# Performance work log

Hardware: AMD Instinct MI355X
Metric: run time of the kernel (lower is better)

Reference implementation:

```python
import jax, jax.numpy as jnp
import numpy as np

H = 512   # span_encoder_hidden_dim == input dim (required by the slicing in forward)
L = 128   # sequence length
B = 4     # batch size


def setup_inputs() -> dict:
    key = jax.random.key(0)
    ks = jax.random.split(key, 7)
    s = 1.0 / np.sqrt(H)
    u = lambda k, shape: jax.random.uniform(k, shape, jnp.float32, -s, s)
    return {
        "word_repr": jax.random.normal(ks[0], (B, L, H), jnp.float32),
        "W_ih_f": u(ks[1], (4 * H, H)),
        "W_hh_f": u(ks[2], (4 * H, H)),
        "b_f": u(ks[3], (4 * H,)),
        "W_ih_b": u(ks[4], (4 * H, H)),
        "W_hh_b": u(ks[5], (4 * H, H)),
        "b_b": u(ks[6], (4 * H,)),
    }


def _lstm(xs, W_ih, W_hh, b):
    # xs: (T, B, D) -> hidden states (T, B, H). PyTorch gate order: i, f, g, o.
    bsz = xs.shape[1]
    hdim = W_hh.shape[1]
    h0 = jnp.zeros((bsz, hdim), xs.dtype)

    def step(carry, xt):
        h, c = carry
        g = xt @ W_ih.T + h @ W_hh.T + b
        gi, gf, gg, go = jnp.split(g, 4, axis=-1)
        c = jax.nn.sigmoid(gf) * c + jax.nn.sigmoid(gi) * jnp.tanh(gg)
        h = jax.nn.sigmoid(go) * jnp.tanh(c)
        return (h, c), h

    _, hs = jax.lax.scan(step, (h0, h0), xs)
    return hs


def reference(word_repr, W_ih_f, W_hh_f, b_f, W_ih_b, W_hh_b, b_b):
    bsz, length, dim = word_repr.shape
    z = jnp.zeros((bsz, 1, dim), word_repr.dtype)
    x = jnp.concatenate([z, word_repr, z], axis=1)      # (B, L+2, D) zero-padded
    xs = jnp.swapaxes(x, 0, 1)                          # (T=L+2, B, D)
    hf = _lstm(xs, W_ih_f, W_hh_f, b_f)                 # forward direction (T, B, H)
    hb = _lstm(xs[::-1], W_ih_b, W_hh_b, b_b)[::-1]     # backward direction (T, B, H)

    Fl = hf[:length]           # forward_repr at positions 0..L-1, (L, B, H)
    Bl = hb[1:length + 1]      # backward_repr at positions 1..L,  (L, B, H)

    # r[i, k] = concat(F[k] - F[i], Bk = B[i+1] - B[k+1]) — fully broadcast, no python loop
    diff_f = Fl[None, :] - Fl[:, None]     # (L, L, B, H)
    diff_b = Bl[:, None] - Bl[None, :]     # (L, L, B, H)
    r = jnp.concatenate([diff_f, diff_b], axis=-1)  # (L, L, B, 2H)

    # original only fills i in [1, L-2], k in [i+1, L-2]; zero elsewhere (torch.empty -> defined zeros)
    ii = jnp.arange(length)[:, None]
    kk = jnp.arange(length)[None, :]
    valid = (ii >= 1) & (kk > ii) & (kk <= length - 2)
    return jnp.where(valid[:, :, None, None], r, jnp.zeros((), r.dtype))
```

## Files before the change

### kernel.cpp

```cpp
#include <hip/hip_runtime.h>
#include <math.h>

#define HH 512
#define LL 128
#define BB 4
#define TT 130
#define G4 2048

#define HF_OFF 0
#define HB_OFF 268288
#define CNT_OFF 536576
#define XPROJ_PER_DIR (TT * BB * G4)
#define XPROJ_OFF (67108864 - 2 * XPROJ_PER_DIR)

__global__ __launch_bounds__(256) void k0_init(float* ws) {
    int tid = threadIdx.x;
    float* HF = ws + HF_OFF;
    float* HB = ws + HB_OFF;
    int* cnt = (int*)(ws + CNT_OFF);
    for (int i = tid; i < G4; i += 256) {
        HF[i] = 0.f;
        HB[(size_t)TT * G4 + i] = 0.f;
    }
    for (int i = tid; i < 2 * 131; i += 256) cnt[i] = 0;
}

__global__ __launch_bounds__(256) void k1_xproj(
    const float* __restrict__ wr,
    const float* __restrict__ WihF, const float* __restrict__ bF,
    const float* __restrict__ WihB, const float* __restrict__ bB,
    float* __restrict__ outbuf) {
    __shared__ float As[16][132];
    __shared__ float Bs[16][132];
    int bid = blockIdx.x;
    int d = bid / 80;
    int r2 = bid % 80;
    int mt = r2 >> 4, nt = r2 & 15;
    const float* Wih  = d ? WihB : WihF;
    const float* bias = d ? bB : bF;
    float* xp = outbuf + XPROJ_OFF + (size_t)d * XPROJ_PER_DIR;
    int tid = threadIdx.x;
    int ty = tid >> 4, tx = tid & 15;
    int m0 = mt * 128, n0 = nt * 128;

    float acc[8][8];
#pragma unroll
    for (int i = 0; i < 8; i++)
#pragma unroll
        for (int j = 0; j < 8; j++) acc[i][j] = 0.f;

    for (int k0 = 0; k0 < HH; k0 += 16) {
#pragma unroll
        for (int l = tid; l < 512; l += 256) {
            int rrow = l & 127;
            int kq = l >> 7;
            int m = m0 + rrow;
            int t = m >> 2, b = m & 3;
            float4 av = make_float4(0.f, 0.f, 0.f, 0.f);
            if (t >= 1 && t <= 128)
                av = *(const float4*)&wr[((size_t)b * LL + (t - 1)) * HH + k0 + kq * 4];
            As[kq * 4 + 0][rrow] = av.x;
            As[kq * 4 + 1][rrow] = av.y;
            As[kq * 4 + 2][rrow] = av.z;
            As[kq * 4 + 3][rrow] = av.w;
            float4 bv = *(const float4*)&Wih[(size_t)(n0 + rrow) * HH + k0 + kq * 4];
            Bs[kq * 4 + 0][rrow] = bv.x;
            Bs[kq * 4 + 1][rrow] = bv.y;
            Bs[kq * 4 + 2][rrow] = bv.z;
            Bs[kq * 4 + 3][rrow] = bv.w;
        }
        __syncthreads();
#pragma unroll
        for (int kk = 0; kk < 16; kk++) {
            float4 a0 = *(const float4*)&As[kk][ty * 8];
            float4 a1 = *(const float4*)&As[kk][ty * 8 + 4];
            float4 b0 = *(const float4*)&Bs[kk][tx * 8];
            float4 b1 = *(const float4*)&Bs[kk][tx * 8 + 4];
            float am[8] = {a0.x, a0.y, a0.z, a0.w, a1.x, a1.y, a1.z, a1.w};
            float bn[8] = {b0.x, b0.y, b0.z, b0.w, b1.x, b1.y, b1.z, b1.w};
#pragma unroll
            for (int i = 0; i < 8; i++)
#pragma unroll
                for (int j = 0; j < 8; j++) acc[i][j] = fmaf(am[i], bn[j], acc[i][j]);
        }
        __syncthreads();
    }
    float4 bv0 = *(const float4*)&bias[n0 + tx * 8];
    float4 bv1 = *(const float4*)&bias[n0 + tx * 8 + 4];
#pragma unroll
    for (int i = 0; i < 8; i++) {
        int m = m0 + ty * 8 + i;
        if (m < TT * BB) {
            float4 o0 = make_float4(acc[i][0] + bv0.x, acc[i][1] + bv0.y,
                                    acc[i][2] + bv0.z, acc[i][3] + bv0.w);
            float4 o1 = make_float4(acc[i][4] + bv1.x, acc[i][5] + bv1.y,
                                    acc[i][6] + bv1.z, acc[i][7] + bv1.w);
            *(float4*)&xp[(size_t)m * G4 + n0 + tx * 8] = o0;
            *(float4*)&xp[(size_t)m * G4 + n0 + tx * 8 + 4] = o1;
        }
    }
}

__device__ __forceinline__ float sigm_(float x) { return 1.f / (1.f + __expf(-x)); }
__device__ __forceinline__ float tanh_(float x) {
    float xc = fminf(fmaxf(x, -15.f), 15.f);
    float e = __expf(-2.f * xc);
    return (1.f - e) / (1.f + e);
}

__global__ __launch_bounds__(256, 1) void k2_lstm(
    const float* __restrict__ WhhF, const float* __restrict__ WhhB,
    const float* __restrict__ outbuf, float* __restrict__ ws) {
    __shared__ float4 hlds4[512];
    __shared__ float g_lds[64][4];
    __shared__ float clds[16][4];

    int bid = blockIdx.x;
    int dir = bid >> 5;
    int g = bid & 31;
    int j0 = g * 16;
    const float* Whh = dir ? WhhB : WhhF;
    const float* xp = outbuf + XPROJ_OFF + (size_t)dir * XPROJ_PER_DIR;
    float* Hbase = ws + (dir ? HB_OFF : HF_OFF);
    int* cnt = (int*)(ws + CNT_OFF) + dir * 131;
    int tid = threadIdx.x;
    int rg = tid >> 5, cc = tid & 31;

    float w[8][16];
#pragma unroll
    for (int i = 0; i < 8; i++) {
        int rl = rg * 8 + i;
        int q = rl >> 4, u = rl & 15;
        const float* wrow = Whh + (size_t)(q * 512 + j0 + u) * HH + cc * 16;
#pragma unroll
        for (int c4 = 0; c4 < 4; c4++) {
            float4 v = *(const float4*)&wrow[c4 * 4];
            w[i][c4 * 4 + 0] = v.x;
            w[i][c4 * 4 + 1] = v.y;
            w[i][c4 * 4 + 2] = v.z;
            w[i][c4 * 4 + 3] = v.w;
        }
    }

    int u_ = (tid >> 2) & 15, b_ = tid & 3;

    for (int s = 0; s < TT; s++) {
        int t = dir ? (129 - s) : s;
        int slot_in = dir ? (t + 1) : t;
        int slot_out = dir ? t : (t + 1);

        float xq[4] = {0.f, 0.f, 0.f, 0.f};
        if (tid < 64) {
#pragma unroll
            for (int q = 0; q < 4; q++)
                xq[q] = xp[((size_t)t * BB + b_) * G4 + q * 512 + j0 + u_];
        }

        if (s > 0) {
            if (tid == 0) {
                while (__hip_atomic_load(&cnt[slot_in], __ATOMIC_RELAXED,
                                         __HIP_MEMORY_SCOPE_AGENT) < 32) {}
            }
            __syncthreads();
            __threadfence();
        }

        const float4* hsrc = (const float4*)(Hbase + (size_t)slot_in * G4);
#pragma unroll
        for (int l = tid; l < 512; l += 256) {
            int brow = l >> 7;
            int quad = l & 127;
            int qs = quad ^ ((quad >> 2) & 7);
            hlds4[brow * 128 + qs] = hsrc[l];
        }
        __syncthreads();

        float p[8][4];
#pragma unroll
        for (int i = 0; i < 8; i++)
#pragma unroll
            for (int b = 0; b < 4; b++) p[i][b] = 0.f;
#pragma unroll
        for (int b = 0; b < 4; b++) {
#pragma unroll
            for (int c4 = 0; c4 < 4; c4++) {
                int quad = cc * 4 + c4;
                int qs = quad ^ (cc & 7);
                float4 h4 = hlds4[b * 128 + qs];
#pragma unroll
                for (int i = 0; i < 8; i++) {
                    p[i][b] = fmaf(w[i][c4 * 4 + 0], h4.x, p[i][b]);
                    p[i][b] = fmaf(w[i][c4 * 4 + 1], h4.y, p[i][b]);
                    p[i][b] = fmaf(w[i][c4 * 4 + 2], h4.z, p[i][b]);
                    p[i][b] = fmaf(w[i][c4 * 4 + 3], h4.w, p[i][b]);
                }
            }
        }
#pragma unroll
        for (int m = 1; m < 32; m <<= 1) {
#pragma unroll
            for (int i = 0; i < 8; i++)
#pragma unroll
                for (int b = 0; b < 4; b++) p[i][b] += __shfl_xor(p[i][b], m, 64);
        }
        if (cc == 0) {
#pragma unroll
            for (int i = 0; i < 8; i++)
#pragma unroll
                for (int b = 0; b < 4; b++) g_lds[rg * 8 + i][b] = p[i][b];
        }
        __syncthreads();

        if (tid < 64) {
            float gv[4];
#pragma unroll
            for (int q = 0; q < 4; q++) gv[q] = g_lds[q * 16 + u_][b_] + xq[q];
            float cprev = (s == 0) ? 0.f : clds[u_][b_];
            float si = sigm_(gv[0]);
            float sf = sigm_(gv[1]);
            float tg = tanh_(gv[2]);
            float so = sigm_(gv[3]);
            float cn = sf * cprev + si * tg;
            clds[u_][b_] = cn;
            Hbase[(size_t)slot_out * G4 + b_ * HH + j0 + u_] = so * tanh_(cn);
        }
        __syncthreads();
        if (tid == 0) {
            __threadfence();
            __hip_atomic_fetch_add(&cnt[slot_out], 1, __ATOMIC_RELEASE,
                                   __HIP_MEMORY_SCOPE_AGENT);
        }
    }
}

__global__ __launch_bounds__(256) void k3_out(const float* __restrict__ ws,
                                              float* __restrict__ out) {
    const float* HF = ws + HF_OFF;
    const float* HB = ws + HB_OFF;
    size_t idx = (size_t)blockIdx.x * 256 + threadIdx.x;
    const size_t total = 16777216;
    const size_t stride = (size_t)2048 * 256;
    for (; idx < total; idx += stride) {
        int c4 = idx & 255;
        int b = (idx >> 8) & 3;
        int k = (idx >> 10) & 127;
        int i = (int)(idx >> 17);
        float4 res = make_float4(0.f, 0.f, 0.f, 0.f);
        if (i >= 1 && k > i && k <= 126) {
            int c0 = c4 * 4;
            if (c0 < 512) {
                float4 a = *(const float4*)&HF[(size_t)(k + 1) * G4 + b * HH + c0];
                float4 c = *(const float4*)&HF[(size_t)(i + 1) * G4 + b * HH + c0];
                res = make_float4(a.x - c.x, a.y - c.y, a.z - c.z, a.w - c.w);
            } else {
                int cd = c0 - 512;
                float4 a = *(const float4*)&HB[(size_t)(i + 1) * G4 + b * HH + cd];
                float4 c = *(const float4*)&HB[(size_t)(k + 1) * G4 + b * HH + cd];
                res = make_float4(a.x - c.x, a.y - c.y, a.z - c.z, a.w - c.w);
            }
        }
        *(float4*)&out[idx * 4] = res;
    }
}

extern "C" void kernel_launch(void* const* d_in, const int* in_sizes, int n_in,
                              void* d_out, int out_size, void* d_ws, size_t ws_size,
                              hipStream_t stream) {
    const float* wr   = (const float*)d_in[0];
    const float* WihF = (const float*)d_in[1];
    const float* WhhF = (const float*)d_in[2];
    const float* bF   = (const float*)d_in[3];
    const float* WihB = (const float*)d_in[4];
    const float* WhhB = (const float*)d_in[5];
    const float* bB   = (const float*)d_in[6];
    float* out = (float*)d_out;
    float* ws = (float*)d_ws;

    k0_init<<<1, 256, 0, stream>>>(ws);
    k1_xproj<<<160, 256, 0, stream>>>(wr, WihF, bF, WihB, bB, out);
    k2_lstm<<<64, 256, 0, stream>>>(WhhF, WhhB, out, ws);
    k3_out<<<2048, 256, 0, stream>>>(ws, out);
}
```

Baseline: 1.678 ms.

## Lighten LSTM recurrence sync, use transpose-reduce, nontemporal output stores

The persistent recurrent kernel drops the __threadfence calls and one __syncthreads per step. It publishes h with relaxed agent-scope atomic stores and reads it back with atomic 64-bit loads, ordering the counter increment with an explicit vmcnt wait. The 32-value butterfly reduction becomes a recursive-halving transpose reduction, so each lane shuffles far fewer values and every lane writes one result. The output kernel switches to nontemporal vector stores so the large output write does not pollute the cache. The weaker memory ordering relies on the vmcnt wait and the relaxed loads being enough for cross-workgroup visibility, which is a correctness risk.

```diff
diff --git a/kernel.cpp b/kernel.cpp
--- a/kernel.cpp
+++ b/kernel.cpp
@@ -6,6 +6,8 @@
 #define BB 4
 #define TT 130
 #define G4 2048
+
+typedef float f32x4_ __attribute__((ext_vector_type(4)));
 
 #define HF_OFF 0
 #define HB_OFF 268288
@@ -134,15 +136,18 @@
         const float* wrow = Whh + (size_t)(q * 512 + j0 + u) * HH + cc * 16;
 #pragma unroll
         for (int c4 = 0; c4 < 4; c4++) {
-            float4 v = *(const float4*)&wrow[c4 * 4];
-            w[i][c4 * 4 + 0] = v.x;
-            w[i][c4 * 4 + 1] = v.y;
-            w[i][c4 * 4 + 2] = v.z;
-            w[i][c4 * 4 + 3] = v.w;
+            float4 vv = *(const float4*)&wrow[c4 * 4];
+            w[i][c4 * 4 + 0] = vv.x;
+            w[i][c4 * 4 + 1] = vv.y;
+            w[i][c4 * 4 + 2] = vv.z;
+            w[i][c4 * 4 + 3] = vv.w;
         }
     }
 
     int u_ = (tid >> 2) & 15, b_ = tid & 3;
+    int brow_s = tid >> 6;
+    int q0 = (2 * tid) & 127;
+    int xw = (q0 >> 2) & 7;
 
     for (int s = 0; s < TT; s++) {
         int t = dir ? (129 - s) : s;
@@ -162,24 +167,27 @@
                                          __HIP_MEMORY_SCOPE_AGENT) < 32) {}
             }
             __syncthreads();
-            __threadfence();
-        }
-
-        const float4* hsrc = (const float4*)(Hbase + (size_t)slot_in * G4);
-#pragma unroll
-        for (int l = tid; l < 512; l += 256) {
-            int brow = l >> 7;
-            int quad = l & 127;
-            int qs = quad ^ ((quad >> 2) & 7);
-            hlds4[brow * 128 + qs] = hsrc[l];
-        }
-        __syncthreads();
-
-        float p[8][4];
-#pragma unroll
-        for (int i = 0; i < 8; i++)
-#pragma unroll
-            for (int b = 0; b < 4; b++) p[i][b] = 0.f;
+        }
+
+        {
+            const unsigned long long* hs =
+                (const unsigned long long*)(Hbase + (size_t)slot_in * G4);
+            unsigned long long u0 = __hip_atomic_load(hs + 4 * tid + 0, __ATOMIC_RELAXED, __HIP_MEMORY_SCOPE_AGENT);
+            unsigned long long u1 = __hip_atomic_load(hs + 4 * tid + 1, __ATOMIC_RELAXED, __HIP_MEMORY_SCOPE_AGENT);
+            unsigned long long u2 = __hip_atomic_load(hs + 4 * tid + 2, __ATOMIC_RELAXED, __HIP_MEMORY_SCOPE_AGENT);
+            unsigned long long u3 = __hip_atomic_load(hs + 4 * tid + 3, __ATOMIC_RELAXED, __HIP_MEMORY_SCOPE_AGENT);
+            float2 f0 = __builtin_bit_cast(float2, u0);
+            float2 f1 = __builtin_bit_cast(float2, u1);
+            float2 f2 = __builtin_bit_cast(float2, u2);
+            float2 f3 = __builtin_bit_cast(float2, u3);
+            hlds4[brow_s * 128 + (q0 ^ xw)] = make_float4(f0.x, f0.y, f1.x, f1.y);
+            hlds4[brow_s * 128 + ((q0 + 1) ^ xw)] = make_float4(f2.x, f2.y, f3.x, f3.y);
+        }
+        __syncthreads();
+
+        float v[32];
+#pragma unroll
+        for (int i = 0; i < 32; i++) v[i] = 0.f;
 #pragma unroll
         for (int b = 0; b < 4; b++) {
 #pragma unroll
@@ -189,26 +197,31 @@
                 float4 h4 = hlds4[b * 128 + qs];
 #pragma unroll
                 for (int i = 0; i < 8; i++) {
-                    p[i][b] = fmaf(w[i][c4 * 4 + 0], h4.x, p[i][b]);
-                    p[i][b] = fmaf(w[i][c4 * 4 + 1], h4.y, p[i][b]);
-                    p[i][b] = fmaf(w[i][c4 * 4 + 2], h4.z, p[i][b]);
-                    p[i][b] = fmaf(w[i][c4 * 4 + 3], h4.w, p[i][b]);
+                    float* pv = &v[i * 4 + b];
+                    *pv = fmaf(w[i][c4 * 4 + 0], h4.x, *pv);
+                    *pv = fmaf(w[i][c4 * 4 + 1], h4.y, *pv);
+                    *pv = fmaf(w[i][c4 * 4 + 2], h4.z, *pv);
+                    *pv = fmaf(w[i][c4 * 4 + 3], h4.w, *pv);
                 }
             }
         }
-#pragma unroll
-        for (int m = 1; m < 32; m <<= 1) {
-#pragma unroll
-            for (int i = 0; i < 8; i++)
-#pragma unroll
-                for (int b = 0; b < 4; b++) p[i][b] += __shfl_xor(p[i][b], m, 64);
-        }
-        if (cc == 0) {
-#pragma unroll
-            for (int i = 0; i < 8; i++)
-#pragma unroll
-                for (int b = 0; b < 4; b++) g_lds[rg * 8 + i][b] = p[i][b];
-        }
+        {
+            int n = 16;
+#pragma unroll
+            for (int m = 16; m >= 1; m >>= 1) {
+                bool up = (cc & m) != 0;
+#pragma unroll
+                for (int j = 0; j < 16; j++) {
+                    if (j < n) {
+                        float send = up ? v[j] : v[j + n];
+                        float recv = __shfl_xor(send, m, 64);
+                        v[j] = (up ? v[j + n] : v[j]) + recv;
+                    }
+                }
+                n >>= 1;
+            }
+        }
+        g_lds[rg * 8 + (cc >> 2)][cc & 3] = v[0];
         __syncthreads();
 
         if (tid < 64) {
@@ -222,12 +235,13 @@
             float so = sigm_(gv[3]);
             float cn = sf * cprev + si * tg;
             clds[u_][b_] = cn;
-            Hbase[(size_t)slot_out * G4 + b_ * HH + j0 + u_] = so * tanh_(cn);
-        }
-        __syncthreads();
+            __hip_atomic_store(&Hbase[(size_t)slot_out * G4 + b_ * HH + j0 + u_],
+                               so * tanh_(cn), __ATOMIC_RELAXED,
+                               __HIP_MEMORY_SCOPE_AGENT);
+        }
         if (tid == 0) {
-            __threadfence();
-            __hip_atomic_fetch_add(&cnt[slot_out], 1, __ATOMIC_RELEASE,
+            asm volatile("s_waitcnt vmcnt(0)" ::: "memory");
+            __hip_atomic_fetch_add(&cnt[slot_out], 1, __ATOMIC_RELAXED,
                                    __HIP_MEMORY_SCOPE_AGENT);
         }
     }
@@ -245,21 +259,21 @@
         int b = (idx >> 8) & 3;
         int k = (idx >> 10) & 127;
         int i = (int)(idx >> 17);
-        float4 res = make_float4(0.f, 0.f, 0.f, 0.f);
+        f32x4_ res = (f32x4_)0.f;
         if (i >= 1 && k > i && k <= 126) {
             int c0 = c4 * 4;
             if (c0 < 512) {
-                float4 a = *(const float4*)&HF[(size_t)(k + 1) * G4 + b * HH + c0];
-                float4 c = *(const float4*)&HF[(size_t)(i + 1) * G4 + b * HH + c0];
-                res = make_float4(a.x - c.x, a.y - c.y, a.z - c.z, a.w - c.w);
+                const f32x4_ a = *(const f32x4_*)&HF[(size_t)(k + 1) * G4 + b * HH + c0];
+                const f32x4_ c = *(const f32x4_*)&HF[(size_t)(i + 1) * G4 + b * HH + c0];
+                res = a - c;
             } else {
                 int cd = c0 - 512;
-                float4 a = *(const float4*)&HB[(size_t)(i + 1) * G4 + b * HH + cd];
-                float4 c = *(const float4*)&HB[(size_t)(k + 1) * G4 + b * HH + cd];
-                res = make_float4(a.x - c.x, a.y - c.y, a.z - c.z, a.w - c.w);
-            }
-        }
-        *(float4*)&out[idx * 4] = res;
+                const f32x4_ a = *(const f32x4_*)&HB[(size_t)(i + 1) * G4 + b * HH + cd];
+                const f32x4_ c = *(const f32x4_*)&HB[(size_t)(k + 1) * G4 + b * HH + cd];
+                res = a - c;
+            }
+        }
+        __builtin_nontemporal_store(res, (f32x4_*)&out[idx * 4]);
     }
 }
 
```

Result: slower. 2.872 ms (+71.2%).
